# Kernel tuning notes

Measured on AMD Instinct MI355X. Metric: run time of the kernel, lower is better.

## Reference

```python
import jax, jax.numpy as jnp
import numpy as np

NU, NI = 100000, 50000          # num_users, num_items
N = NU + NI                      # total nodes
D = 64                           # hidden_dim
DE = 16                          # eigs_dim
L = 2                            # n_layers
E = 1500000                      # edges per layer
NP = 14                          # 2**(sample_hop+1)-2 path types
EPS = 1e-5


def setup_inputs() -> dict:
    key = jax.random.key(0)
    ks = jax.random.split(key, 7)
    return {
        "user_emb": jax.random.normal(ks[0], (NU, D), jnp.float32) * 0.1,
        "item_emb": jax.random.normal(ks[1], (NI, D), jnp.float32) * 0.1,
        "eigs": jax.random.normal(ks[2], (N, DE), jnp.float32),
        "lambda0": jax.random.normal(ks[3], (L,), jnp.float32) * 0.1,
        "path_w": jax.random.normal(ks[4], (L, NP), jnp.float32) * 0.1,
        "indices": jax.random.randint(ks[5], (L, 2, E), 0, N),
        "path_type": jax.random.randint(ks[6], (L, E), 0, NP),
    }


def _layer_norm(x):
    mu = x.mean(-1, keepdims=True)
    var = ((x - mu) ** 2).mean(-1, keepdims=True)
    return (x - mu) * jax.lax.rsqrt(var + EPS)


def _sparse_softmax(row, vals, n):
    # torch: clamp(exp(v), min=-5, max=5) -> effectively min(exp(v), 5)
    e = jnp.clip(jnp.exp(vals), -5.0, 5.0)
    s = jax.ops.segment_sum(e, row, num_segments=n)
    s = jnp.where(s == 0.0, 1.0, s)
    return e / s[row]


def _encoder(x, idx, pt, eigs, lam, pw):
    y = _layer_norm(x)                                   # [N, D]
    r, c = idx[0], idx[1]                                # [E]
    yc = y[c]                                            # [E, D]
    xs = (y[r] * yc).sum(-1) * (1.0 / jnp.sqrt(jnp.float32(D)))  # [E]
    ys = (eigs[r] * eigs[c]).sum(-1)                     # [E]
    s0 = _sparse_softmax(r, xs + jnp.exp(lam) * ys, N)
    s1 = _sparse_softmax(r, pw[pt], N)
    s = 0.5 * (s0 + s1)                                  # mean over the two scores
    # SpMM: out[r] += s_e * y[c_e]
    return jax.ops.segment_sum(s[:, None] * yc, r, num_segments=N)


def reference(user_emb, item_emb, eigs, lambda0, path_w, indices, path_type):
    x = jnp.concatenate([user_emb, item_emb], axis=0)    # [N, D]
    embs = [x]
    for l in range(L):
        x = _encoder(x, indices[l], path_type[l], eigs, lambda0[l], path_w[l])
        embs.append(x)
    return jnp.mean(jnp.stack(embs, axis=1), axis=1)      # [N, D]
```

## Files before the change

kernel.cpp:

```cpp
#include <hip/hip_runtime.h>
#include <hip/hip_bf16.h>

#define NUSERS 100000
#define NITEMS 50000
#define NN 150000
#define DD 64
#define DE 16
#define NLAYERS 2
#define NE 1500000
#define NPATH 14
#define LN_EPS 1e-5f

#define BROWS 512
#define NBUK 293
#define NB (2 * NBUK)
#define CHUNK 4096
#define NCHUNK ((NE + CHUNK - 1) / CHUNK)
#define LEN (2 * NBUK * NCHUNK)
#define SCAN_BLK 1024
#define NSCB ((LEN + SCAN_BLK - 1) / SCAN_BLK)

__device__ __forceinline__ float blo(unsigned u) {
    union { unsigned q; float f; } v; v.q = u << 16; return v.f;
}
__device__ __forceinline__ float bhi(unsigned u) {
    union { unsigned q; float f; } v; v.q = u & 0xffff0000u; return v.f;
}

__global__ void k_ln(const float* __restrict__ uemb,
                     const float* __restrict__ iemb,
                     const float* __restrict__ xin,
                     float* __restrict__ acc,
                     unsigned short* __restrict__ y,
                     int first) {
    int row = blockIdx.x * 4 + (threadIdx.x >> 6);
    int lane = threadIdx.x & 63;
    if (row >= NN) return;
    int i = row * DD + lane;
    float v;
    if (first) {
        v = (row < NUSERS) ? uemb[i] : iemb[i - NUSERS * DD];
        acc[i] = v;
    } else {
        v = xin[i];
        acc[i] += v;
    }
    float s = v;
    #pragma unroll
    for (int m = 32; m; m >>= 1) s += __shfl_xor(s, m, 64);
    float mu = s * (1.0f / 64.0f);
    float d = v - mu;
    float q = d * d;
    #pragma unroll
    for (int m = 32; m; m >>= 1) q += __shfl_xor(q, m, 64);
    float var = q * (1.0f / 64.0f);
    float yn = d * rsqrtf(var + LN_EPS);
    __hip_bfloat16 h = __float2bfloat16(yn);
    y[i] = *reinterpret_cast<unsigned short*>(&h);
}

__global__ void k_pcount(const int* __restrict__ idx, int* __restrict__ cntmat) {
    int blk = blockIdx.x;
    int layer = blk / NCHUNK;
    int k = blk - layer * NCHUNK;
    __shared__ int h[NBUK];
    for (int t = threadIdx.x; t < NBUK; t += 256) h[t] = 0;
    __syncthreads();
    const int* rrow = idx + (size_t)layer * 2 * NE;
    int base = k * CHUNK;
    int lim = min(CHUNK, NE - base);
    for (int j = threadIdx.x; j < lim; j += 256)
        atomicAdd(&h[rrow[base + j] >> 9], 1);
    __syncthreads();
    for (int t = threadIdx.x; t < NBUK; t += 256)
        cntmat[((size_t)layer * NBUK + t) * NCHUNK + k] = h[t];
}

__global__ __launch_bounds__(SCAN_BLK) void k_scan1(
        const int* __restrict__ cnt, int* __restrict__ off,
        int* __restrict__ bsum, int n) {
    __shared__ int sm[SCAN_BLK];
    int t = threadIdx.x;
    int i = blockIdx.x * SCAN_BLK + t;
    int v = (i < n) ? cnt[i] : 0;
    sm[t] = v;
    __syncthreads();
    #pragma unroll
    for (int d = 1; d < SCAN_BLK; d <<= 1) {
        int a = (t >= d) ? sm[t - d] : 0;
        __syncthreads();
        sm[t] += a;
        __syncthreads();
    }
    if (i < n) off[i] = sm[t] - v;
    if (t == SCAN_BLK - 1) bsum[blockIdx.x] = sm[t];
}

__global__ void k_scan2(int* __restrict__ bsum, int nb) {
    __shared__ int sm[256];
    int t = threadIdx.x;
    int v = (t < nb) ? bsum[t] : 0;
    sm[t] = v;
    __syncthreads();
    #pragma unroll
    for (int d = 1; d < 256; d <<= 1) {
        int a = (t >= d) ? sm[t - d] : 0;
        __syncthreads();
        sm[t] += a;
        __syncthreads();
    }
    if (t < nb) bsum[t] = sm[t] - v;
}

__global__ __launch_bounds__(SCAN_BLK) void k_scan3(
        int* __restrict__ off, const int* __restrict__ bsum,
        int* __restrict__ bstart, int n) {
    int i = blockIdx.x * SCAN_BLK + threadIdx.x;
    if (i == 0) bstart[NB] = 2 * NE;
    if (i >= n) return;
    int v = off[i] + bsum[blockIdx.x];
    off[i] = v;
    if (i % NCHUNK == 0) bstart[i / NCHUNK] = v;
}

__global__ void k_pscatter(const int* __restrict__ idx,
                           const int* __restrict__ ptyp,
                           const int* __restrict__ exsc,
                           unsigned int* __restrict__ stage) {
    int blk = blockIdx.x;
    int layer = blk / NCHUNK;
    int k = blk - layer * NCHUNK;
    __shared__ int hofs[NBUK];
    for (int t = threadIdx.x; t < NBUK; t += 256)
        hofs[t] = exsc[((size_t)layer * NBUK + t) * NCHUNK + k];
    __syncthreads();
    const int* rrow = idx + (size_t)layer * 2 * NE;
    const int* ccol = rrow + NE;
    const int* pp   = ptyp + (size_t)layer * NE;
    int base = k * CHUNK;
    int lim = min(CHUNK, NE - base);
    for (int j = threadIdx.x; j < lim; j += 256) {
        int e = base + j;
        int r = rrow[e];
        int pos = atomicAdd(&hofs[r >> 9], 1);
        stage[pos] = (unsigned)ccol[e] | ((unsigned)pp[e] << 18)
                   | ((unsigned)(r & 511) << 22);
    }
}

__global__ __launch_bounds__(1024) void k_bscatter(
        const unsigned int* __restrict__ stage,
        const int* __restrict__ bstart,
        int* __restrict__ csv,
        int2* __restrict__ roff) {
    __shared__ int scnt[BROWS];
    __shared__ int scur[BROWS];
    int b = blockIdx.x;
    int t = threadIdx.x;
    int layer = b / NBUK;
    int brow0 = (b - layer * NBUK) * BROWS;
    int nrows = min(BROWS, NN - brow0);
    int start = bstart[b];
    int n = bstart[b + 1] - start;
    if (t < BROWS) scnt[t] = 0;
    __syncthreads();
    for (int p = t; p < n; p += 1024)
        atomicAdd(&scnt[stage[start + p] >> 22], 1);
    __syncthreads();
    int orig = (t < BROWS) ? scnt[t] : 0;
    #pragma unroll
    for (int d = 1; d < BROWS; d <<= 1) {
        int a = 0;
        if (t < BROWS && t >= d) a = scnt[t - d];
        __syncthreads();
        if (t < BROWS) scnt[t] += a;
        __syncthreads();
    }
    if (t < BROWS) {
        int excl = scnt[t] - orig;
        scur[t] = excl;
        if (t < nrows)
            roff[(size_t)layer * NN + brow0 + t] =
                make_int2(start + excl, start + excl + orig);
    }
    __syncthreads();
    for (int p = t; p < n; p += 1024) {
        unsigned rec = stage[start + p];
        int pos = atomicAdd(&scur[rec >> 22], 1);
        csv[start + pos] = (int)(rec & 0x3fffffu);
    }
}

__global__ void k_row(const unsigned short* __restrict__ y,
                      const float* __restrict__ eigs,
                      const int2* __restrict__ roff,
                      const int* __restrict__ csv,
                      const float* __restrict__ pw,
                      const float* __restrict__ lam,
                      int layer,
                      const float* __restrict__ accin,
                      float* __restrict__ xout) {
    __shared__ float pexp[NPATH];
    __shared__ float selam;
    int t = threadIdx.x;
    if (t < NPATH) pexp[t] = fminf(expf(pw[layer * NPATH + t]), 5.0f);
    if (t == NPATH) selam = expf(lam[layer]);
    __syncthreads();

    int row = blockIdx.x * 4 + (t >> 6);
    int lane = t & 63;
    int g = lane >> 3;
    int sl = lane & 7;
    int2 pr = roff[row];
    int p0 = pr.x, p1 = pr.y;

    uint4 ar = reinterpret_cast<const uint4*>(y + (size_t)row * DD)[sl];
    float a0 = blo(ar.x), a1 = bhi(ar.x), a2 = blo(ar.y), a3 = bhi(ar.y);
    float a4 = blo(ar.z), a5 = bhi(ar.z), a6 = blo(ar.w), a7 = bhi(ar.w);
    float2 er = reinterpret_cast<const float2*>(eigs + (size_t)row * DE)[sl];
    float elam = selam;

    float sum0 = 0.f, sum1 = 0.f;
    float A0=0,A1=0,A2=0,A3=0,A4=0,A5=0,A6=0,A7=0;
    float B0=0,B1=0,B2=0,B3=0,B4=0,B5=0,B6=0,B7=0;

    for (int p = p0; p < p1; p += 8) {
        int q = p + g;
        bool ok = q < p1;
        int rec = 0;
        uint4 bv = make_uint4(0u, 0u, 0u, 0u);
        float2 ec = make_float2(0.f, 0.f);
        if (ok) {
            rec = csv[q];
            int c = rec & 0x3ffff;
            bv = reinterpret_cast<const uint4*>(y + (size_t)c * DD)[sl];
            ec = reinterpret_cast<const float2*>(eigs + (size_t)c * DE)[sl];
        }
        float b0 = blo(bv.x), b1 = bhi(bv.x), b2 = blo(bv.y), b3 = bhi(bv.y);
        float b4 = blo(bv.z), b5 = bhi(bv.z), b6 = blo(bv.w), b7 = bhi(bv.w);
        float px = a0*b0 + a1*b1 + a2*b2 + a3*b3
                 + a4*b4 + a5*b5 + a6*b6 + a7*b7;
        float pv = er.x * ec.x + er.y * ec.y;
        float sc = px * 0.125f + elam * pv;
        sc += __shfl_xor(sc, 4, 64);
        sc += __shfl_xor(sc, 2, 64);
        sc += __shfl_xor(sc, 1, 64);
        float e0 = ok ? fminf(expf(sc), 5.0f) : 0.f;
        float e1 = ok ? pexp[(rec >> 18) & 0xF] : 0.f;
        sum0 += e0; sum1 += e1;
        A0 += e0*b0; A1 += e0*b1; A2 += e0*b2; A3 += e0*b3;
        A4 += e0*b4; A5 += e0*b5; A6 += e0*b6; A7 += e0*b7;
        B0 += e1*b0; B1 += e1*b1; B2 += e1*b2; B3 += e1*b3;
        B4 += e1*b4; B5 += e1*b5; B6 += e1*b6; B7 += e1*b7;
    }

    #pragma unroll
    for (int m = 8; m <= 32; m <<= 1) {
        sum0 += __shfl_xor(sum0, m, 64);
        sum1 += __shfl_xor(sum1, m, 64);
    }
    float rinv0 = 0.5f / ((sum0 == 0.f) ? 1.f : sum0);
    float rinv1 = 0.5f / ((sum1 == 0.f) ? 1.f : sum1);

    float o0 = rinv0*A0 + rinv1*B0, o1 = rinv0*A1 + rinv1*B1;
    float o2 = rinv0*A2 + rinv1*B2, o3 = rinv0*A3 + rinv1*B3;
    float o4 = rinv0*A4 + rinv1*B4, o5 = rinv0*A5 + rinv1*B5;
    float o6 = rinv0*A6 + rinv1*B6, o7 = rinv0*A7 + rinv1*B7;
    #pragma unroll
    for (int m = 8; m <= 32; m <<= 1) {
        o0 += __shfl_xor(o0, m, 64); o1 += __shfl_xor(o1, m, 64);
        o2 += __shfl_xor(o2, m, 64); o3 += __shfl_xor(o3, m, 64);
        o4 += __shfl_xor(o4, m, 64); o5 += __shfl_xor(o5, m, 64);
        o6 += __shfl_xor(o6, m, 64); o7 += __shfl_xor(o7, m, 64);
    }
    if (g == 0) {
        float* dst = xout + (size_t)row * DD + sl * 8;
        if (accin) {
            const float* ap = accin + (size_t)row * DD + sl * 8;
            o0 = (o0 + ap[0]) * (1.f/3.f); o1 = (o1 + ap[1]) * (1.f/3.f);
            o2 = (o2 + ap[2]) * (1.f/3.f); o3 = (o3 + ap[3]) * (1.f/3.f);
            o4 = (o4 + ap[4]) * (1.f/3.f); o5 = (o5 + ap[5]) * (1.f/3.f);
            o6 = (o6 + ap[6]) * (1.f/3.f); o7 = (o7 + ap[7]) * (1.f/3.f);
        }
        reinterpret_cast<float4*>(dst)[0] = make_float4(o0, o1, o2, o3);
        reinterpret_cast<float4*>(dst)[1] = make_float4(o4, o5, o6, o7);
    }
}

extern "C" void kernel_launch(void* const* d_in, const int* in_sizes, int n_in,
                              void* d_out, int out_size, void* d_ws, size_t ws_size,
                              hipStream_t stream) {
    const float* uemb = (const float*)d_in[0];
    const float* iemb = (const float*)d_in[1];
    const float* eigs = (const float*)d_in[2];
    const float* lam  = (const float*)d_in[3];
    const float* pw   = (const float*)d_in[4];
    const int* idx    = (const int*)d_in[5];
    const int* ptyp   = (const int*)d_in[6];

    char* w = (char*)d_ws;
    unsigned int* stage  = (unsigned int*)(w);
    int*          cnt    = (int*)(w + 12000000);
    int*          off    = (int*)(w + 12860248);
    int*          bsum   = (int*)(w + 13720496);
    int*          bstart = (int*)(w + 13721344);
    float*          acc  = (float*)(w);
    float*          x    = (float*)(w + 38400000);
    unsigned short* y    = (unsigned short*)(w + 76800000);
    int*            csv  = (int*)(w + 96000000);
    int2*           roff = (int2*)(w + 108000000);

    const int gRows = NN / 4;

    k_pcount<<<2 * NCHUNK, 256, 0, stream>>>(idx, cnt);
    k_scan1<<<NSCB, SCAN_BLK, 0, stream>>>(cnt, off, bsum, LEN);
    k_scan2<<<1, 256, 0, stream>>>(bsum, NSCB);
    k_scan3<<<NSCB, SCAN_BLK, 0, stream>>>(off, bsum, bstart, LEN);
    k_pscatter<<<2 * NCHUNK, 256, 0, stream>>>(idx, ptyp, off, stage);
    k_bscatter<<<NB, 1024, 0, stream>>>(stage, bstart, csv, roff);

    k_ln<<<gRows, 256, 0, stream>>>(uemb, iemb, nullptr, acc, y, 1);
    k_row<<<gRows, 256, 0, stream>>>(y, eigs, roff, csv, pw, lam, 0,
                                     nullptr, x);
    k_ln<<<gRows, 256, 0, stream>>>(nullptr, nullptr, x, acc, y, 0);
    k_row<<<gRows, 256, 0, stream>>>(y, eigs, roff + NN, csv, pw, lam, 1,
                                     acc, (float*)d_out);
}
```

Measured before the change: 442.5 us.

## Fuse layernorm into SpMM epilogue, bf16 eigs, restructure bucket scan

The second layernorm pass moves into the layer-0 row kernel epilogue, which now writes the bf16 normalized embeddings directly. The running-sum accumulator buffer goes away because the final output reads the original embeddings and x1 instead. Eigenvectors are converted once to bf16 to halve the gather bytes per edge, and the three-kernel global scan becomes a per-bucket scan plus a small total scan whose offsets are added in the scatter. This trades some precision on the eigenvector scores for fewer kernel launches and less memory traffic.

```diff
diff --git a/kernel.cpp b/kernel.cpp
--- a/kernel.cpp
+++ b/kernel.cpp
@@ -6,7 +6,6 @@
 #define NN 150000
 #define DD 64
 #define DE 16
-#define NLAYERS 2
 #define NE 1500000
 #define NPATH 14
 #define LN_EPS 1e-5f
@@ -16,9 +15,6 @@
 #define NB (2 * NBUK)
 #define CHUNK 4096
 #define NCHUNK ((NE + CHUNK - 1) / CHUNK)
-#define LEN (2 * NBUK * NCHUNK)
-#define SCAN_BLK 1024
-#define NSCB ((LEN + SCAN_BLK - 1) / SCAN_BLK)
 
 __device__ __forceinline__ float blo(unsigned u) {
     union { unsigned q; float f; } v; v.q = u << 16; return v.f;
@@ -26,25 +22,25 @@
 __device__ __forceinline__ float bhi(unsigned u) {
     union { unsigned q; float f; } v; v.q = u & 0xffff0000u; return v.f;
 }
-
-__global__ void k_ln(const float* __restrict__ uemb,
-                     const float* __restrict__ iemb,
-                     const float* __restrict__ xin,
-                     float* __restrict__ acc,
-                     unsigned short* __restrict__ y,
-                     int first) {
+__device__ __forceinline__ unsigned f2b(float f) {
+    union { float f; unsigned u; } v; v.f = f;
+    return (v.u + 0x7fffu + ((v.u >> 16) & 1u)) >> 16;
+}
+
+__global__ void k_eig(const float* __restrict__ eigs,
+                      unsigned short* __restrict__ e16) {
+    int i = blockIdx.x * 256 + threadIdx.x;
+    if (i < NN * DE) e16[i] = (unsigned short)f2b(eigs[i]);
+}
+
+__global__ void k_ln0(const float* __restrict__ uemb,
+                      const float* __restrict__ iemb,
+                      unsigned short* __restrict__ y) {
     int row = blockIdx.x * 4 + (threadIdx.x >> 6);
     int lane = threadIdx.x & 63;
     if (row >= NN) return;
     int i = row * DD + lane;
-    float v;
-    if (first) {
-        v = (row < NUSERS) ? uemb[i] : iemb[i - NUSERS * DD];
-        acc[i] = v;
-    } else {
-        v = xin[i];
-        acc[i] += v;
-    }
+    float v = (row < NUSERS) ? uemb[i] : iemb[i - NUSERS * DD];
     float s = v;
     #pragma unroll
     for (int m = 32; m; m >>= 1) s += __shfl_xor(s, m, 64);
@@ -53,10 +49,8 @@
     float q = d * d;
     #pragma unroll
     for (int m = 32; m; m >>= 1) q += __shfl_xor(q, m, 64);
-    float var = q * (1.0f / 64.0f);
-    float yn = d * rsqrtf(var + LN_EPS);
-    __hip_bfloat16 h = __float2bfloat16(yn);
-    y[i] = *reinterpret_cast<unsigned short*>(&h);
+    float rs = rsqrtf(q * (1.0f / 64.0f) + LN_EPS);
+    y[i] = (unsigned short)f2b(d * rs);
 }
 
 __global__ void k_pcount(const int* __restrict__ idx, int* __restrict__ cntmat) {
@@ -76,63 +70,57 @@
         cntmat[((size_t)layer * NBUK + t) * NCHUNK + k] = h[t];
 }
 
-__global__ __launch_bounds__(SCAN_BLK) void k_scan1(
-        const int* __restrict__ cnt, int* __restrict__ off,
-        int* __restrict__ bsum, int n) {
-    __shared__ int sm[SCAN_BLK];
+__global__ __launch_bounds__(512) void k_bukscan(const int* __restrict__ cnt,
+                                                 int* __restrict__ exsc,
+                                                 int* __restrict__ tot) {
+    __shared__ int sm[512];
+    int b = blockIdx.x;
     int t = threadIdx.x;
-    int i = blockIdx.x * SCAN_BLK + t;
-    int v = (i < n) ? cnt[i] : 0;
+    int v = (t < NCHUNK) ? cnt[(size_t)b * NCHUNK + t] : 0;
     sm[t] = v;
     __syncthreads();
     #pragma unroll
-    for (int d = 1; d < SCAN_BLK; d <<= 1) {
+    for (int d = 1; d < 512; d <<= 1) {
         int a = (t >= d) ? sm[t - d] : 0;
         __syncthreads();
         sm[t] += a;
         __syncthreads();
     }
-    if (i < n) off[i] = sm[t] - v;
-    if (t == SCAN_BLK - 1) bsum[blockIdx.x] = sm[t];
-}
-
-__global__ void k_scan2(int* __restrict__ bsum, int nb) {
-    __shared__ int sm[256];
+    if (t < NCHUNK) exsc[(size_t)b * NCHUNK + t] = sm[t] - v;
+    if (t == 511) tot[b] = sm[511];
+}
+
+__global__ __launch_bounds__(1024) void k_totscan(const int* __restrict__ tot,
+                                                  int* __restrict__ bstart) {
+    __shared__ int sm[1024];
     int t = threadIdx.x;
-    int v = (t < nb) ? bsum[t] : 0;
+    int v = (t < NB) ? tot[t] : 0;
     sm[t] = v;
     __syncthreads();
     #pragma unroll
-    for (int d = 1; d < 256; d <<= 1) {
+    for (int d = 1; d < 1024; d <<= 1) {
         int a = (t >= d) ? sm[t - d] : 0;
         __syncthreads();
         sm[t] += a;
         __syncthreads();
     }
-    if (t < nb) bsum[t] = sm[t] - v;
-}
-
-__global__ __launch_bounds__(SCAN_BLK) void k_scan3(
-        int* __restrict__ off, const int* __restrict__ bsum,
-        int* __restrict__ bstart, int n) {
-    int i = blockIdx.x * SCAN_BLK + threadIdx.x;
-    if (i == 0) bstart[NB] = 2 * NE;
-    if (i >= n) return;
-    int v = off[i] + bsum[blockIdx.x];
-    off[i] = v;
-    if (i % NCHUNK == 0) bstart[i / NCHUNK] = v;
+    if (t < NB) bstart[t] = sm[t] - v;
+    if (t == 0) bstart[NB] = 2 * NE;
 }
 
 __global__ void k_pscatter(const int* __restrict__ idx,
                            const int* __restrict__ ptyp,
                            const int* __restrict__ exsc,
+                           const int* __restrict__ bstart,
                            unsigned int* __restrict__ stage) {
     int blk = blockIdx.x;
     int layer = blk / NCHUNK;
     int k = blk - layer * NCHUNK;
     __shared__ int hofs[NBUK];
-    for (int t = threadIdx.x; t < NBUK; t += 256)
-        hofs[t] = exsc[((size_t)layer * NBUK + t) * NCHUNK + k];
+    for (int t = threadIdx.x; t < NBUK; t += 256) {
+        int b = layer * NBUK + t;
+        hofs[t] = bstart[b] + exsc[(size_t)b * NCHUNK + k];
+    }
     __syncthreads();
     const int* rrow = idx + (size_t)layer * 2 * NE;
     const int* ccol = rrow + NE;
@@ -192,14 +180,17 @@
 }
 
 __global__ void k_row(const unsigned short* __restrict__ y,
-                      const float* __restrict__ eigs,
+                      const unsigned short* __restrict__ e16,
                       const int2* __restrict__ roff,
                       const int* __restrict__ csv,
                       const float* __restrict__ pw,
                       const float* __restrict__ lam,
                       int layer,
-                      const float* __restrict__ accin,
-                      float* __restrict__ xout) {
+                      const float* __restrict__ uemb,
+                      const float* __restrict__ iemb,
+                      float* __restrict__ x1,
+                      unsigned short* __restrict__ y1,
+                      float* __restrict__ out) {
     __shared__ float pexp[NPATH];
     __shared__ float selam;
     int t = threadIdx.x;
@@ -217,7 +208,8 @@
     uint4 ar = reinterpret_cast<const uint4*>(y + (size_t)row * DD)[sl];
     float a0 = blo(ar.x), a1 = bhi(ar.x), a2 = blo(ar.y), a3 = bhi(ar.y);
     float a4 = blo(ar.z), a5 = bhi(ar.z), a6 = blo(ar.w), a7 = bhi(ar.w);
-    float2 er = reinterpret_cast<const float2*>(eigs + (size_t)row * DE)[sl];
+    unsigned eru = reinterpret_cast<const unsigned*>(e16 + (size_t)row * DE)[sl];
+    float er0 = blo(eru), er1 = bhi(eru);
     float elam = selam;
 
     float sum0 = 0.f, sum1 = 0.f;
@@ -229,18 +221,18 @@
         bool ok = q < p1;
         int rec = 0;
         uint4 bv = make_uint4(0u, 0u, 0u, 0u);
-        float2 ec = make_float2(0.f, 0.f);
+        unsigned ecu = 0u;
         if (ok) {
             rec = csv[q];
             int c = rec & 0x3ffff;
             bv = reinterpret_cast<const uint4*>(y + (size_t)c * DD)[sl];
-            ec = reinterpret_cast<const float2*>(eigs + (size_t)c * DE)[sl];
+            ecu = reinterpret_cast<const unsigned*>(e16 + (size_t)c * DE)[sl];
         }
         float b0 = blo(bv.x), b1 = bhi(bv.x), b2 = blo(bv.y), b3 = bhi(bv.y);
         float b4 = blo(bv.z), b5 = bhi(bv.z), b6 = blo(bv.w), b7 = bhi(bv.w);
         float px = a0*b0 + a1*b1 + a2*b2 + a3*b3
                  + a4*b4 + a5*b5 + a6*b6 + a7*b7;
-        float pv = er.x * ec.x + er.y * ec.y;
+        float pv = er0 * blo(ecu) + er1 * bhi(ecu);
         float sc = px * 0.125f + elam * pv;
         sc += __shfl_xor(sc, 4, 64);
         sc += __shfl_xor(sc, 2, 64);
@@ -274,16 +266,47 @@
         o6 += __shfl_xor(o6, m, 64); o7 += __shfl_xor(o7, m, 64);
     }
     if (g == 0) {
-        float* dst = xout + (size_t)row * DD + sl * 8;
-        if (accin) {
-            const float* ap = accin + (size_t)row * DD + sl * 8;
-            o0 = (o0 + ap[0]) * (1.f/3.f); o1 = (o1 + ap[1]) * (1.f/3.f);
-            o2 = (o2 + ap[2]) * (1.f/3.f); o3 = (o3 + ap[3]) * (1.f/3.f);
-            o4 = (o4 + ap[4]) * (1.f/3.f); o5 = (o5 + ap[5]) * (1.f/3.f);
-            o6 = (o6 + ap[6]) * (1.f/3.f); o7 = (o7 + ap[7]) * (1.f/3.f);
+        int ofs = sl * 8;
+        if (layer == 0) {
+            float* dst = x1 + (size_t)row * DD + ofs;
+            reinterpret_cast<float4*>(dst)[0] = make_float4(o0, o1, o2, o3);
+            reinterpret_cast<float4*>(dst)[1] = make_float4(o4, o5, o6, o7);
+            float s = o0+o1+o2+o3+o4+o5+o6+o7;
+            s += __shfl_xor(s, 1, 64);
+            s += __shfl_xor(s, 2, 64);
+            s += __shfl_xor(s, 4, 64);
+            float mu = s * (1.0f / 64.0f);
+            float d0=o0-mu, d1=o1-mu, d2=o2-mu, d3=o3-mu;
+            float d4=o4-mu, d5=o5-mu, d6=o6-mu, d7=o7-mu;
+            float qv = d0*d0+d1*d1+d2*d2+d3*d3+d4*d4+d5*d5+d6*d6+d7*d7;
+            qv += __shfl_xor(qv, 1, 64);
+            qv += __shfl_xor(qv, 2, 64);
+            qv += __shfl_xor(qv, 4, 64);
+            float rs = rsqrtf(qv * (1.0f / 64.0f) + LN_EPS);
+            uint4 pk;
+            pk.x = f2b(d0*rs) | (f2b(d1*rs) << 16);
+            pk.y = f2b(d2*rs) | (f2b(d3*rs) << 16);
+            pk.z = f2b(d4*rs) | (f2b(d5*rs) << 16);
+            pk.w = f2b(d6*rs) | (f2b(d7*rs) << 16);
+            reinterpret_cast<uint4*>(y1 + (size_t)row * DD)[sl] = pk;
+        } else {
+            const float* e = (row < NUSERS)
+                ? (uemb + (size_t)row * DD + ofs)
+                : (iemb + (size_t)(row - NUSERS) * DD + ofs);
+            const float* xp = x1 + (size_t)row * DD + ofs;
+            float4 ea = reinterpret_cast<const float4*>(e)[0];
+            float4 eb = reinterpret_cast<const float4*>(e)[1];
+            float4 xa = reinterpret_cast<const float4*>(xp)[0];
+            float4 xb = reinterpret_cast<const float4*>(xp)[1];
+            float* dst = out + (size_t)row * DD + ofs;
+            const float k3 = 1.0f / 3.0f;
+            reinterpret_cast<float4*>(dst)[0] = make_float4(
+                (ea.x + xa.x + o0) * k3, (ea.y + xa.y + o1) * k3,
+                (ea.z + xa.z + o2) * k3, (ea.w + xa.w + o3) * k3);
+            reinterpret_cast<float4*>(dst)[1] = make_float4(
+                (eb.x + xb.x + o4) * k3, (eb.y + xb.y + o5) * k3,
+                (eb.z + xb.z + o6) * k3, (eb.w + xb.w + o7) * k3);
         }
-        reinterpret_cast<float4*>(dst)[0] = make_float4(o0, o1, o2, o3);
-        reinterpret_cast<float4*>(dst)[1] = make_float4(o4, o5, o6, o7);
     }
 }
 
@@ -299,30 +322,31 @@
     const int* ptyp   = (const int*)d_in[6];
 
     char* w = (char*)d_ws;
-    unsigned int* stage  = (unsigned int*)(w);
-    int*          cnt    = (int*)(w + 12000000);
-    int*          off    = (int*)(w + 12860248);
-    int*          bsum   = (int*)(w + 13720496);
-    int*          bstart = (int*)(w + 13721344);
-    float*          acc  = (float*)(w);
-    float*          x    = (float*)(w + 38400000);
-    unsigned short* y    = (unsigned short*)(w + 76800000);
-    int*            csv  = (int*)(w + 96000000);
-    int2*           roff = (int2*)(w + 108000000);
+    float*          x1     = (float*)(w);
+    unsigned short* y0     = (unsigned short*)(w + 38400000);
+    unsigned short* y1     = (unsigned short*)(w + 57600000);
+    int*            csv    = (int*)(w + 76800000);
+    int2*           roff   = (int2*)(w + 88800000);
+    unsigned short* e16    = (unsigned short*)(w + 91200000);
+    unsigned int*   stage  = (unsigned int*)(w + 96000000);
+    int*            cnt    = (int*)(w + 108000000);
+    int*            exsc   = (int*)(w + 108860248);
+    int*            tot    = (int*)(w + 109720496);
+    int*            bstart = (int*)(w + 109722840);
 
     const int gRows = NN / 4;
 
     k_pcount<<<2 * NCHUNK, 256, 0, stream>>>(idx, cnt);
-    k_scan1<<<NSCB, SCAN_BLK, 0, stream>>>(cnt, off, bsum, LEN);
-    k_scan2<<<1, 256, 0, stream>>>(bsum, NSCB);
-    k_scan3<<<NSCB, SCAN_BLK, 0, stream>>>(off, bsum, bstart, LEN);
-    k_pscatter<<<2 * NCHUNK, 256, 0, stream>>>(idx, ptyp, off, stage);
+    k_bukscan<<<NB, 512, 0, stream>>>(cnt, exsc, tot);
+    k_totscan<<<1, 1024, 0, stream>>>(tot, bstart);
+    k_pscatter<<<2 * NCHUNK, 256, 0, stream>>>(idx, ptyp, exsc, bstart, stage);
     k_bscatter<<<NB, 1024, 0, stream>>>(stage, bstart, csv, roff);
 
-    k_ln<<<gRows, 256, 0, stream>>>(uemb, iemb, nullptr, acc, y, 1);
-    k_row<<<gRows, 256, 0, stream>>>(y, eigs, roff, csv, pw, lam, 0,
-                                     nullptr, x);
-    k_ln<<<gRows, 256, 0, stream>>>(nullptr, nullptr, x, acc, y, 0);
-    k_row<<<gRows, 256, 0, stream>>>(y, eigs, roff + NN, csv, pw, lam, 1,
-                                     acc, (float*)d_out);
-}
+    k_eig<<<(NN * DE + 255) / 256, 256, 0, stream>>>(eigs, e16);
+    k_ln0<<<gRows, 256, 0, stream>>>(uemb, iemb, y0);
+
+    k_row<<<gRows, 256, 0, stream>>>(y0, e16, roff, csv, pw, lam, 0,
+                                     nullptr, nullptr, x1, y1, nullptr);
+    k_row<<<gRows, 256, 0, stream>>>(y1, e16, roff + NN, csv, pw, lam, 1,
+                                     uemb, iemb, x1, nullptr, (float*)d_out);
+}
```

New measurement: 424.9 us. -4.0%, faster.
